# Kernel optimization log

Measured on AMD Instinct MI355X. Metric: run time of the kernel, lower is better.

Reference implementation:

```python
import jax, jax.numpy as jnp
import numpy as np

B, N, NODE_DIM = 8, 128, 64
L, RES_DIM = 512, 1024
CG, CP = 128, 128
NUM_GNN_STEPS = 3
HID = CG + CP // 2  # interaction hidden = 192


def setup_inputs() -> dict:
    key = jax.random.key(0)
    ks = jax.random.split(key, 20)
    a = (jax.random.uniform(ks[0], (B, N, N)) < 0.05).astype(jnp.float32)
    adj = jnp.clip(a + jnp.swapaxes(a, 1, 2), 0.0, 1.0)
    adj = adj * (1.0 - jnp.eye(N, dtype=jnp.float32))
    nodes = jax.random.normal(ks[1], (B, N, NODE_DIM), dtype=jnp.float32)
    prot = jax.random.normal(ks[2], (B, L, RES_DIM), dtype=jnp.float32)
    s = 0.02
    inp = {
        "adj_mats": adj, "nodes": nodes, "protein_sequences": prot,
        "Wn": jax.random.normal(ks[3], (NODE_DIM, CG)) * s, "bn": jnp.zeros((CG,)),
        "Wg": jax.random.normal(ks[4], (CG, CG)) * s, "bg": jnp.zeros((CG,)),
        "Wr": jax.random.normal(ks[5], (RES_DIM, CP)) * s, "br": jnp.zeros((CP,)),
        "Wa": jax.random.normal(ks[6], (CG + CP, 1)) * s, "ba": jnp.zeros((1,)),
        "W1": jax.random.normal(ks[7], (CG + CP, HID)) * s, "b1": jnp.zeros((HID,)),
        "W2": jax.random.normal(ks[8], (HID, CG)) * s, "b2": jnp.zeros((CG,)),
        "Wo": jax.random.normal(ks[9], (CG, 1)) * s, "bo": jnp.zeros((1,)),
    }
    return inp


def reference(adj_mats, nodes, protein_sequences,
              Wn, bn, Wg, bg, Wr, br, Wa, ba, W1, b1, W2, b2, Wo, bo):
    # node compression: [B,N,CG]
    h = nodes @ Wn + bn
    deg = jnp.clip(jnp.sum(adj_mats, axis=-1), 1.0, None)        # [B,N]
    norm = deg ** -0.5                                           # [B,N]
    for i in range(NUM_GNN_STEPS):
        m = jnp.einsum('bij,bjc->bic', adj_mats, h * norm[..., None])
        h = (m * norm[..., None]) @ Wg + bg
        h = jnp.tanh(h) if i == NUM_GNN_STEPS - 1 else jax.nn.relu(h)
    # residue compression: [B,L,CP]
    r = protein_sequences @ Wr + br
    # MergeSnE1: all-pairs broadcast concat -> [B, N*L, CG+CP]
    cat = jnp.concatenate([
        jnp.broadcast_to(h[:, :, None, :], (B, N, L, CG)),
        jnp.broadcast_to(r[:, None, :, :], (B, N, L, CP)),
    ], axis=-1).reshape(B, N * L, CG + CP)
    # attention: Linear -> Softmax over last dim (size 1 => all ones, faithful)
    attn = jax.nn.softmax(cat @ Wa + ba, axis=-1)                # [B,N*L,1]
    inter = jax.nn.relu(cat @ W1 + b1) @ W2 + b2                 # [B,N*L,CG]
    weighted_sum = jnp.sum(attn * inter, axis=1)                 # [B,CG]
    return weighted_sum @ Wo + bo                                # [B,1]
```

## Files before the change

kernel.cpp:

```cpp
#include <hip/hip_runtime.h>
#include <hip/hip_bf16.h>

#define BB 8
#define NN 128
#define ND 64
#define LL 512
#define RD 1024
#define CG 128
#define HID 192

typedef __attribute__((ext_vector_type(8))) short short8;
typedef __attribute__((ext_vector_type(4))) float f32x4;

__device__ __forceinline__ unsigned short f2bf(float x) {
    return __bfloat16_as_ushort(__float2bfloat16(x));
}
__device__ __forceinline__ float bf2f(unsigned short h) {
    unsigned u = ((unsigned)h) << 16;
    return __builtin_bit_cast(float, u);
}
__device__ __forceinline__ float fast_tanh(float x) {
    float e = __expf(2.0f * x);
    return 1.0f - 2.0f * __builtin_amdgcn_rcpf(e + 1.0f);
}
#define MFMA __builtin_amdgcn_mfma_f32_16x16x32_bf16

__global__ __launch_bounds__(512, 1) void k1(
    const float* __restrict__ Wr, const float* __restrict__ br,
    const float* __restrict__ W1, const float* __restrict__ b1,
    const float* __restrict__ Wg, const float* __restrict__ Wn,
    const float* __restrict__ W2, const float* __restrict__ b2,
    const float* __restrict__ Wo, const float* __restrict__ bo,
    unsigned short* __restrict__ WcT, float* __restrict__ vbuf,
    float* __restrict__ b1cg, float* __restrict__ out,
    unsigned short* __restrict__ WgTg, unsigned short* __restrict__ W1Tg,
    unsigned short* __restrict__ WnTg)
{
    __shared__ unsigned short W1T[HID][136];
    int t = threadIdx.x, blk = blockIdx.x;
    int w = t >> 6, l = t & 63, lr = l & 15, ks = l >> 4, lk = ks * 8;
    const float* W1b = W1 + CG * HID;

    if (blk < 16) {
        int r0 = blk * 64;
        #pragma unroll
        for (int q = 0; q < 48; ++q) {
            int e = t + 512 * q;
            int m = e / HID, c = e % HID;
            W1T[c][m] = f2bf(W1[(size_t)(CG + m) * HID + c]);
        }
        int rt = w & 3, jh = w >> 2;
        short8 awr[4];
        #pragma unroll
        for (int kk = 0; kk < 4; ++kk) {
            const float* wp = Wr + (size_t)(r0 + rt * 16 + lr) * CG + kk * 32 + lk;
            float4 q0 = *(const float4*)wp;
            float4 q1 = *(const float4*)(wp + 4);
            unsigned short u[8];
            u[0]=f2bf(q0.x); u[1]=f2bf(q0.y); u[2]=f2bf(q0.z); u[3]=f2bf(q0.w);
            u[4]=f2bf(q1.x); u[5]=f2bf(q1.y); u[6]=f2bf(q1.z); u[7]=f2bf(q1.w);
            awr[kk] = *(const short8*)u;
        }
        __syncthreads();
        #pragma unroll
        for (int jt6 = 0; jt6 < 6; ++jt6) {
            int jt = jh * 6 + jt6;
            f32x4 d = {0.f, 0.f, 0.f, 0.f};
            #pragma unroll
            for (int kk = 0; kk < 4; ++kk) {
                short8 bf = *(const short8*)(&W1T[jt * 16 + lr][kk * 32 + lk]);
                d = MFMA(awr[kk], bf, d, 0, 0, 0);
            }
            unsigned short u[4];
            #pragma unroll
            for (int i = 0; i < 4; ++i) u[i] = f2bf(d[i]);
            *(uint2*)(WcT + (size_t)(jt * 16 + lr) * RD + r0 + rt * 16 + ks * 4) = *(uint2*)u;
        }
        return;
    }
    if (blk == 16) {
        if (t < HID) {
            float s = 0.f;
            #pragma unroll 8
            for (int k = 0; k < CG; ++k) s = fmaf(W2[t * CG + k], Wo[k], s);
            vbuf[t] = s;
        }
        if (t < BB) {
            float s = 0.f;
            for (int k = 0; k < CG; ++k) s = fmaf(b2[k], Wo[k], s);
            out[t] = (float)(NN * LL) * s + bo[0];
        }
        if (t >= 192 && t < 384) {
            int j = t - 192;
            float s = b1[j];
            #pragma unroll 8
            for (int m = 0; m < CG; ++m)
                s = fmaf(br[m], W1b[(size_t)m * HID + j], s);
            b1cg[j] = s;
        }
        return;
    }
    if (blk < 21) {
        int c = (blk - 17) * 32 + (t >> 4);
        int j8 = (t & 15) * 8;
        unsigned short u[8];
        #pragma unroll
        for (int q = 0; q < 8; ++q)
            u[q] = f2bf(Wg[(size_t)(j8 + q) * CG + c]);
        *(short8*)(WgTg + (size_t)c * CG + j8) = *(const short8*)u;
        return;
    }
    if (blk < 24) {
        int jj0 = (blk - 21) * 64;
        #pragma unroll
        for (int qq = 0; qq < 2; ++qq) {
            int u8 = t + 512 * qq;
            int jj = jj0 + (u8 >> 4);
            int k8 = (u8 & 15) * 8;
            unsigned short u[8];
            #pragma unroll
            for (int q = 0; q < 8; ++q)
                u[q] = f2bf(W1[(size_t)(k8 + q) * HID + jj]);
            *(short8*)(W1Tg + (size_t)jj * CG + k8) = *(const short8*)u;
        }
        return;
    }
    #pragma unroll
    for (int qq = 0; qq < 2; ++qq) {
        int u8 = t + 512 * qq;
        int c = u8 >> 3;
        int k8 = (u8 & 7) * 8;
        unsigned short u[8];
        #pragma unroll
        for (int q = 0; q < 8; ++q)
            u[q] = f2bf(Wn[(size_t)(k8 + q) * CG + c]);
        *(short8*)(WnTg + (size_t)c * ND + k8) = *(const short8*)u;
    }
}

__global__ __launch_bounds__(512, 1) void k_gnn(
    const float* __restrict__ adj, const float* __restrict__ nodes,
    const unsigned short* __restrict__ WnTg, const float* __restrict__ bn,
    const unsigned short* __restrict__ WgTg, const float* __restrict__ bg,
    const unsigned short* __restrict__ W1Tg, const float* __restrict__ b1cg,
    unsigned short* __restrict__ hW1b)
{
    __shared__ unsigned short hT[NN][136];
    __shared__ unsigned short mbuf[NN][72];
    __shared__ unsigned short WgT[NN][136];
    __shared__ unsigned short W1T[HID][136];
    __shared__ float snorm[NN];
    __shared__ float b1cL[HID];
    __shared__ float sbg[NN];
    int t = threadIdx.x, blk = blockIdx.x;
    int w = t >> 6, l = t & 63, lr = l & 15, ks = l >> 4, lk = ks * 8;
    int b = blk;
    int i0 = w * 16;

    {
        float* dscr = (float*)&mbuf[0][0];
        int row = t >> 2, q4 = t & 3;
        const float* ar = adj + ((size_t)b * NN + row) * NN + q4 * 32;
        float d = 0.f;
        #pragma unroll
        for (int c4 = 0; c4 < 8; ++c4) {
            float4 p = *(const float4*)(ar + c4 * 4);
            d += (p.x + p.y) + (p.z + p.w);
        }
        dscr[row * 4 + q4] = d;
        __syncthreads();
        if (t < NN) {
            snorm[t] = rsqrtf(fmaxf(dscr[t*4] + dscr[t*4+1] + dscr[t*4+2] + dscr[t*4+3], 1.f));
        } else if (t < 320) {
            b1cL[t - 128] = b1cg[t - 128];
        } else if (t < 448) {
            sbg[t - 320] = bg[t - 320];
        }
        __syncthreads();
    }

    unsigned short* WnT = &mbuf[0][0];
    #pragma unroll
    for (int qq = 0; qq < 2; ++qq) {
        int u8 = t + 512 * qq;
        int c = u8 >> 3, k8 = (u8 & 7) * 8;
        *(short8*)(WnT + c * 72 + k8) = *(const short8*)(WnTg + (size_t)c * ND + k8);
    }
    #pragma unroll
    for (int qq = 0; qq < 4; ++qq) {
        int u8 = t + 512 * qq;
        int c = u8 >> 4, j8 = (u8 & 15) * 8;
        *(short8*)(&WgT[c][j8]) = *(const short8*)(WgTg + (size_t)c * CG + j8);
    }
    #pragma unroll
    for (int qq = 0; qq < 6; ++qq) {
        int u8 = t + 512 * qq;
        int jj = u8 >> 4, k8 = (u8 & 15) * 8;
        *(short8*)(&W1T[jj][k8]) = *(const short8*)(W1Tg + (size_t)jj * CG + k8);
    }

    short8 af[4];
    {
        float ni = snorm[i0 + lr];
        const float* ar = adj + ((size_t)b * NN + i0 + lr) * NN;
        #pragma unroll
        for (int kk = 0; kk < 4; ++kk) {
            int kb = kk * 32 + lk;
            float4 p0 = *(const float4*)(ar + kb);
            float4 p1 = *(const float4*)(ar + kb + 4);
            unsigned short u[8];
            u[0] = f2bf(p0.x * ni * snorm[kb+0]); u[1] = f2bf(p0.y * ni * snorm[kb+1]);
            u[2] = f2bf(p0.z * ni * snorm[kb+2]); u[3] = f2bf(p0.w * ni * snorm[kb+3]);
            u[4] = f2bf(p1.x * ni * snorm[kb+4]); u[5] = f2bf(p1.y * ni * snorm[kb+5]);
            u[6] = f2bf(p1.z * ni * snorm[kb+6]); u[7] = f2bf(p1.w * ni * snorm[kb+7]);
            af[kk] = *(const short8*)u;
        }
    }
    short8 bnod[2];
    #pragma unroll
    for (int kk = 0; kk < 2; ++kk) {
        const float* np = nodes + ((size_t)b * NN + i0 + lr) * ND + kk * 32 + lk;
        float4 q0 = *(const float4*)np;
        float4 q1 = *(const float4*)(np + 4);
        unsigned short u[8];
        u[0]=f2bf(q0.x); u[1]=f2bf(q0.y); u[2]=f2bf(q0.z); u[3]=f2bf(q0.w);
        u[4]=f2bf(q1.x); u[5]=f2bf(q1.y); u[6]=f2bf(q1.z); u[7]=f2bf(q1.w);
        bnod[kk] = *(const short8*)u;
    }
    __syncthreads();

    #pragma unroll
    for (int ct = 0; ct < 8; ++ct) {
        f32x4 d = {0.f, 0.f, 0.f, 0.f};
        #pragma unroll
        for (int kk = 0; kk < 2; ++kk) {
            short8 afw = *(const short8*)(WnT + (ct * 16 + lr) * 72 + kk * 32 + lk);
            d = MFMA(afw, bnod[kk], d, 0, 0, 0);
        }
        #pragma unroll
        for (int i = 0; i < 4; ++i)
            hT[ct * 16 + ks * 4 + i][i0 + lr] = f2bf(d[i] + bn[ct * 16 + ks * 4 + i]);
    }
    __syncthreads();

    for (int s = 0; s < 3; ++s) {
        f32x4 acc8[8];
        #pragma unroll
        for (int ct = 0; ct < 8; ++ct) acc8[ct] = (f32x4){0.f, 0.f, 0.f, 0.f};
        #pragma unroll
        for (int hf = 0; hf < 2; ++hf) {
            #pragma unroll
            for (int jt = 0; jt < 4; ++jt) {
                int jg = hf * 64 + jt * 16;
                f32x4 d = {0.f, 0.f, 0.f, 0.f};
                #pragma unroll
                for (int kk = 0; kk < 4; ++kk) {
                    short8 bf = *(const short8*)(&hT[jg + lr][kk * 32 + lk]);
                    d = MFMA(af[kk], bf, d, 0, 0, 0);
                }
                #pragma unroll
                for (int i = 0; i < 4; ++i)
                    mbuf[i0 + ks * 4 + i][jt * 16 + lr] = f2bf(d[i]);
            }
            short8 bm[2];
            #pragma unroll
            for (int kk = 0; kk < 2; ++kk)
                bm[kk] = *(const short8*)(&mbuf[i0 + lr][kk * 32 + lk]);
            #pragma unroll
            for (int ct = 0; ct < 8; ++ct) {
                #pragma unroll
                for (int kk = 0; kk < 2; ++kk) {
                    short8 wf = *(const short8*)(&WgT[ct * 16 + lr][hf * 64 + kk * 32 + lk]);
                    if (s < 2)
                        acc8[ct] = MFMA(wf, bm[kk], acc8[ct], 0, 0, 0);
                    else
                        acc8[ct] = MFMA(bm[kk], wf, acc8[ct], 0, 0, 0);
                }
            }
        }
        __syncthreads();
        if (s < 2) {
            #pragma unroll
            for (int ct = 0; ct < 8; ++ct)
                #pragma unroll
                for (int i = 0; i < 4; ++i)
                    hT[ct * 16 + ks * 4 + i][i0 + lr] =
                        f2bf(fmaxf(acc8[ct][i] + sbg[ct * 16 + ks * 4 + i], 0.f));
        } else {
            #pragma unroll
            for (int ct = 0; ct < 8; ++ct)
                #pragma unroll
                for (int i = 0; i < 4; ++i)
                    hT[i0 + ks * 4 + i][ct * 16 + lr] =
                        f2bf(fast_tanh(acc8[ct][i] + sbg[ct * 16 + lr]));
        }
        __syncthreads();
    }

    {
        short8 bh[4];
        #pragma unroll
        for (int kk = 0; kk < 4; ++kk)
            bh[kk] = *(const short8*)(&hT[i0 + lr][kk * 32 + lk]);
        #pragma unroll
        for (int jjt = 0; jjt < 12; ++jjt) {
            f32x4 d = {0.f, 0.f, 0.f, 0.f};
            #pragma unroll
            for (int kk = 0; kk < 4; ++kk) {
                short8 wf = *(const short8*)(&W1T[jjt * 16 + lr][kk * 32 + lk]);
                d = MFMA(wf, bh[kk], d, 0, 0, 0);
            }
            #pragma unroll
            for (int i = 0; i < 4; ++i) {
                int jj = jjt * 16 + ks * 4 + i;
                hW1b[(size_t)b * HID * NN + jj * NN + i0 + lr] = f2bf(d[i] + b1cL[jj]);
            }
        }
    }
}

__global__ __launch_bounds__(512, 4) void k_gemm(
    const float* __restrict__ prot, const unsigned short* __restrict__ WcT,
    const unsigned short* __restrict__ hW1b, const float* __restrict__ vbuf,
    float* __restrict__ out)
{
    __shared__ unsigned short aT[16 * 1032];
    __shared__ unsigned short h1[HID * 136];
    __shared__ float pbuf[2 * 16 * 192];
    __shared__ float sred[8];
    int t = threadIdx.x, blk = blockIdx.x;
    int b = blk >> 5, lc = blk & 31;
    int w = t >> 6, l = t & 63, lr = l & 15, ks = l >> 4, lk = ks * 8;
    int w2 = w >> 2, wj = w & 3;

    #pragma unroll
    for (int q = 0; q < 4; ++q) {
        int e = t + 512 * q;
        int row = e >> 7;
        int c8 = (e & 127) * 8;
        const float* pr = prot + ((size_t)(b * LL + lc * 16 + row)) * RD + c8;
        float4 p0 = *(const float4*)pr;
        float4 p1 = *(const float4*)(pr + 4);
        unsigned short u[8];
        u[0]=f2bf(p0.x); u[1]=f2bf(p0.y); u[2]=f2bf(p0.z); u[3]=f2bf(p0.w);
        u[4]=f2bf(p1.x); u[5]=f2bf(p1.y); u[6]=f2bf(p1.z); u[7]=f2bf(p1.w);
        *(short8*)(aT + row * 1032 + c8) = *(const short8*)u;
    }
    #pragma unroll
    for (int q = 0; q < 6; ++q) {
        int u8 = t + 512 * q;
        int row = u8 >> 4;
        int n8 = (u8 & 15) * 8;
        short8 v = *(const short8*)(hW1b + (size_t)b * HID * NN + row * NN + n8);
        *(short8*)(h1 + row * 136 + n8) = v;
    }
    float v0 = vbuf[wj * 48 + lr];
    float v1 = vbuf[wj * 48 + 16 + lr];
    float v2 = vbuf[wj * 48 + 32 + lr];
    __syncthreads();

    f32x4 a0 = {0.f,0.f,0.f,0.f}, a1 = a0, a2 = a0;
    {
        const unsigned short* ap = aT + lr * 1032 + w2 * 512 + lk;
        const unsigned short* bp = WcT + (size_t)(wj * 48 + lr) * RD + w2 * 512 + lk;
        #pragma unroll 4
        for (int k0 = 0; k0 < 512; k0 += 32) {
            short8 av = *(const short8*)(ap + k0);
            short8 b0 = *(const short8*)(bp + k0);
            short8 b1 = *(const short8*)(bp + 16 * RD + k0);
            short8 b2 = *(const short8*)(bp + 32 * RD + k0);
            a0 = MFMA(av, b0, a0, 0, 0, 0);
            a1 = MFMA(av, b1, a1, 0, 0, 0);
            a2 = MFMA(av, b2, a2, 0, 0, 0);
        }
    }
    #pragma unroll
    for (int i = 0; i < 4; ++i) {
        int r = ks * 4 + i;
        pbuf[(w2 * 16 + r) * 192 + wj * 48 + lr]      = a0[i];
        pbuf[(w2 * 16 + r) * 192 + wj * 48 + 16 + lr] = a1[i];
        pbuf[(w2 * 16 + r) * 192 + wj * 48 + 32 + lr] = a2[i];
    }
    __syncthreads();
    float rw0[4], rw1[4], rw2[4];
    #pragma unroll
    for (int i = 0; i < 4; ++i) {
        int r = ks * 4 + i;
        rw0[i] = pbuf[r * 192 + wj*48 + lr]      + pbuf[(16 + r) * 192 + wj*48 + lr];
        rw1[i] = pbuf[r * 192 + wj*48 + 16 + lr] + pbuf[(16 + r) * 192 + wj*48 + 16 + lr];
        rw2[i] = pbuf[r * 192 + wj*48 + 32 + lr] + pbuf[(16 + r) * 192 + wj*48 + 32 + lr];
    }

    const unsigned short* h0p = h1 + (wj * 48 + lr) * 136 + w2 * 64;
    const unsigned short* h1p = h0p + 16 * 136;
    const unsigned short* h2p = h0p + 32 * 136;
    float s = 0.f;
    #pragma unroll 2
    for (int n0 = 0; n0 < 64; n0 += 4) {
        unsigned short e0[4], e1[4], e2[4];
        *(uint2*)e0 = *(const uint2*)(h0p + n0);
        *(uint2*)e1 = *(const uint2*)(h1p + n0);
        *(uint2*)e2 = *(const uint2*)(h2p + n0);
        #pragma unroll
        for (int q = 0; q < 4; ++q) {
            float hh0 = bf2f(e0[q]), hh1 = bf2f(e1[q]), hh2 = bf2f(e2[q]);
            #pragma unroll
            for (int i = 0; i < 4; ++i) {
                s = fmaf(v0, fmaxf(rw0[i] + hh0, 0.f), s);
                s = fmaf(v1, fmaxf(rw1[i] + hh1, 0.f), s);
                s = fmaf(v2, fmaxf(rw2[i] + hh2, 0.f), s);
            }
        }
    }
    for (int off = 32; off; off >>= 1) s += __shfl_down(s, off);
    if (l == 0) sred[w] = s;
    __syncthreads();
    if (t == 0) {
        float tot = ((sred[0] + sred[1]) + (sred[2] + sred[3]))
                  + ((sred[4] + sred[5]) + (sred[6] + sred[7]));
        atomicAdd(&out[b], tot);
    }
}

extern "C" void kernel_launch(void* const* d_in, const int* in_sizes, int n_in,
                              void* d_out, int out_size, void* d_ws, size_t ws_size,
                              hipStream_t stream)
{
    const float* adj   = (const float*)d_in[0];
    const float* nodes = (const float*)d_in[1];
    const float* prot  = (const float*)d_in[2];
    const float* Wn    = (const float*)d_in[3];
    const float* bn    = (const float*)d_in[4];
    const float* Wg    = (const float*)d_in[5];
    const float* bg    = (const float*)d_in[6];
    const float* Wr    = (const float*)d_in[7];
    const float* br    = (const float*)d_in[8];
    const float* W1    = (const float*)d_in[11];
    const float* b1    = (const float*)d_in[12];
    const float* W2    = (const float*)d_in[13];
    const float* b2    = (const float*)d_in[14];
    const float* Wo    = (const float*)d_in[15];
    const float* bo    = (const float*)d_in[16];

    float* ws     = (float*)d_ws;
    float* vbuf   = ws;
    float* b1cg   = ws + 192;
    unsigned short* hW1b = (unsigned short*)(ws + 384);
    unsigned short* WcT  = hW1b + (size_t)BB * HID * NN;
    unsigned short* WgTg = WcT + (size_t)HID * RD;
    unsigned short* W1Tg = WgTg + CG * CG;
    unsigned short* WnTg = W1Tg + HID * CG;
    float* out    = (float*)d_out;

    hipLaunchKernelGGL(k1, dim3(25), dim3(512), 0, stream,
                       Wr, br, W1, b1, Wg, Wn, W2, b2, Wo, bo,
                       WcT, vbuf, b1cg, out, WgTg, W1Tg, WnTg);
    hipLaunchKernelGGL(k_gnn, dim3(8), dim3(512), 0, stream,
                       adj, nodes, WnTg, bn, WgTg, bg, W1Tg, b1cg, hW1b);
    hipLaunchKernelGGL(k_gemm, dim3(256), dim3(512), 0, stream,
                       prot, WcT, hW1b, vbuf, out);
}
```

Baseline: 56.69 us.

## Merge GNN and projection GEMM kernels with flag-based inter-block synchronization

Fuses the GNN kernel and the protein GEMM kernel into one 256-block launch. Blocks 248-255 run the GNN per batch and publish a release flag. The other blocks first compute their protein projection tiles, with blocks 0-7 also taking the tiles normally owned by the GNN blocks, then spin on the flag before consuming hW1b. The aim is to overlap the serial GNN with the bandwidth-heavy GEMM and drop one launch. The cost is spin-waiting, a dependence on all blocks being co-resident to avoid deadlock, and a heavier load on blocks 0-7.

Result: slower. 70.35 us (+24.1%).

```diff
diff --git a/kernel.cpp b/kernel.cpp
--- a/kernel.cpp
+++ b/kernel.cpp
@@ -34,7 +34,7 @@
     unsigned short* __restrict__ WcT, float* __restrict__ vbuf,
     float* __restrict__ b1cg, float* __restrict__ out,
     unsigned short* __restrict__ WgTg, unsigned short* __restrict__ W1Tg,
-    unsigned short* __restrict__ WnTg)
+    unsigned short* __restrict__ WnTg, unsigned* __restrict__ flags)
 {
     __shared__ unsigned short W1T[HID][136];
     int t = threadIdx.x, blk = blockIdx.x;
@@ -98,6 +98,7 @@
                 s = fmaf(br[m], W1b[(size_t)m * HID + j], s);
             b1cg[j] = s;
         }
+        if (t >= 384) flags[t - 384] = 0u;
         return;
     }
     if (blk < 21) {
@@ -138,201 +139,9 @@
     }
 }
 
-__global__ __launch_bounds__(512, 1) void k_gnn(
-    const float* __restrict__ adj, const float* __restrict__ nodes,
-    const unsigned short* __restrict__ WnTg, const float* __restrict__ bn,
-    const unsigned short* __restrict__ WgTg, const float* __restrict__ bg,
-    const unsigned short* __restrict__ W1Tg, const float* __restrict__ b1cg,
-    unsigned short* __restrict__ hW1b)
-{
-    __shared__ unsigned short hT[NN][136];
-    __shared__ unsigned short mbuf[NN][72];
-    __shared__ unsigned short WgT[NN][136];
-    __shared__ unsigned short W1T[HID][136];
-    __shared__ float snorm[NN];
-    __shared__ float b1cL[HID];
-    __shared__ float sbg[NN];
-    int t = threadIdx.x, blk = blockIdx.x;
-    int w = t >> 6, l = t & 63, lr = l & 15, ks = l >> 4, lk = ks * 8;
-    int b = blk;
-    int i0 = w * 16;
-
-    {
-        float* dscr = (float*)&mbuf[0][0];
-        int row = t >> 2, q4 = t & 3;
-        const float* ar = adj + ((size_t)b * NN + row) * NN + q4 * 32;
-        float d = 0.f;
-        #pragma unroll
-        for (int c4 = 0; c4 < 8; ++c4) {
-            float4 p = *(const float4*)(ar + c4 * 4);
-            d += (p.x + p.y) + (p.z + p.w);
-        }
-        dscr[row * 4 + q4] = d;
-        __syncthreads();
-        if (t < NN) {
-            snorm[t] = rsqrtf(fmaxf(dscr[t*4] + dscr[t*4+1] + dscr[t*4+2] + dscr[t*4+3], 1.f));
-        } else if (t < 320) {
-            b1cL[t - 128] = b1cg[t - 128];
-        } else if (t < 448) {
-            sbg[t - 320] = bg[t - 320];
-        }
-        __syncthreads();
-    }
-
-    unsigned short* WnT = &mbuf[0][0];
-    #pragma unroll
-    for (int qq = 0; qq < 2; ++qq) {
-        int u8 = t + 512 * qq;
-        int c = u8 >> 3, k8 = (u8 & 7) * 8;
-        *(short8*)(WnT + c * 72 + k8) = *(const short8*)(WnTg + (size_t)c * ND + k8);
-    }
-    #pragma unroll
-    for (int qq = 0; qq < 4; ++qq) {
-        int u8 = t + 512 * qq;
-        int c = u8 >> 4, j8 = (u8 & 15) * 8;
-        *(short8*)(&WgT[c][j8]) = *(const short8*)(WgTg + (size_t)c * CG + j8);
-    }
-    #pragma unroll
-    for (int qq = 0; qq < 6; ++qq) {
-        int u8 = t + 512 * qq;
-        int jj = u8 >> 4, k8 = (u8 & 15) * 8;
-        *(short8*)(&W1T[jj][k8]) = *(const short8*)(W1Tg + (size_t)jj * CG + k8);
-    }
-
-    short8 af[4];
-    {
-        float ni = snorm[i0 + lr];
-        const float* ar = adj + ((size_t)b * NN + i0 + lr) * NN;
-        #pragma unroll
-        for (int kk = 0; kk < 4; ++kk) {
-            int kb = kk * 32 + lk;
-            float4 p0 = *(const float4*)(ar + kb);
-            float4 p1 = *(const float4*)(ar + kb + 4);
-            unsigned short u[8];
-            u[0] = f2bf(p0.x * ni * snorm[kb+0]); u[1] = f2bf(p0.y * ni * snorm[kb+1]);
-            u[2] = f2bf(p0.z * ni * snorm[kb+2]); u[3] = f2bf(p0.w * ni * snorm[kb+3]);
-            u[4] = f2bf(p1.x * ni * snorm[kb+4]); u[5] = f2bf(p1.y * ni * snorm[kb+5]);
-            u[6] = f2bf(p1.z * ni * snorm[kb+6]); u[7] = f2bf(p1.w * ni * snorm[kb+7]);
-            af[kk] = *(const short8*)u;
-        }
-    }
-    short8 bnod[2];
-    #pragma unroll
-    for (int kk = 0; kk < 2; ++kk) {
-        const float* np = nodes + ((size_t)b * NN + i0 + lr) * ND + kk * 32 + lk;
-        float4 q0 = *(const float4*)np;
-        float4 q1 = *(const float4*)(np + 4);
-        unsigned short u[8];
-        u[0]=f2bf(q0.x); u[1]=f2bf(q0.y); u[2]=f2bf(q0.z); u[3]=f2bf(q0.w);
-        u[4]=f2bf(q1.x); u[5]=f2bf(q1.y); u[6]=f2bf(q1.z); u[7]=f2bf(q1.w);
-        bnod[kk] = *(const short8*)u;
-    }
-    __syncthreads();
-
-    #pragma unroll
-    for (int ct = 0; ct < 8; ++ct) {
-        f32x4 d = {0.f, 0.f, 0.f, 0.f};
-        #pragma unroll
-        for (int kk = 0; kk < 2; ++kk) {
-            short8 afw = *(const short8*)(WnT + (ct * 16 + lr) * 72 + kk * 32 + lk);
-            d = MFMA(afw, bnod[kk], d, 0, 0, 0);
-        }
-        #pragma unroll
-        for (int i = 0; i < 4; ++i)
-            hT[ct * 16 + ks * 4 + i][i0 + lr] = f2bf(d[i] + bn[ct * 16 + ks * 4 + i]);
-    }
-    __syncthreads();
-
-    for (int s = 0; s < 3; ++s) {
-        f32x4 acc8[8];
-        #pragma unroll
-        for (int ct = 0; ct < 8; ++ct) acc8[ct] = (f32x4){0.f, 0.f, 0.f, 0.f};
-        #pragma unroll
-        for (int hf = 0; hf < 2; ++hf) {
-            #pragma unroll
-            for (int jt = 0; jt < 4; ++jt) {
-                int jg = hf * 64 + jt * 16;
-                f32x4 d = {0.f, 0.f, 0.f, 0.f};
-                #pragma unroll
-                for (int kk = 0; kk < 4; ++kk) {
-                    short8 bf = *(const short8*)(&hT[jg + lr][kk * 32 + lk]);
-                    d = MFMA(af[kk], bf, d, 0, 0, 0);
-                }
-                #pragma unroll
-                for (int i = 0; i < 4; ++i)
-                    mbuf[i0 + ks * 4 + i][jt * 16 + lr] = f2bf(d[i]);
-            }
-            short8 bm[2];
-            #pragma unroll
-            for (int kk = 0; kk < 2; ++kk)
-                bm[kk] = *(const short8*)(&mbuf[i0 + lr][kk * 32 + lk]);
-            #pragma unroll
-            for (int ct = 0; ct < 8; ++ct) {
-                #pragma unroll
-                for (int kk = 0; kk < 2; ++kk) {
-                    short8 wf = *(const short8*)(&WgT[ct * 16 + lr][hf * 64 + kk * 32 + lk]);
-                    if (s < 2)
-                        acc8[ct] = MFMA(wf, bm[kk], acc8[ct], 0, 0, 0);
-                    else
-                        acc8[ct] = MFMA(bm[kk], wf, acc8[ct], 0, 0, 0);
-                }
-            }
-        }
-        __syncthreads();
-        if (s < 2) {
-            #pragma unroll
-            for (int ct = 0; ct < 8; ++ct)
-                #pragma unroll
-                for (int i = 0; i < 4; ++i)
-                    hT[ct * 16 + ks * 4 + i][i0 + lr] =
-                        f2bf(fmaxf(acc8[ct][i] + sbg[ct * 16 + ks * 4 + i], 0.f));
-        } else {
-            #pragma unroll
-            for (int ct = 0; ct < 8; ++ct)
-                #pragma unroll
-                for (int i = 0; i < 4; ++i)
-                    hT[i0 + ks * 4 + i][ct * 16 + lr] =
-                        f2bf(fast_tanh(acc8[ct][i] + sbg[ct * 16 + lr]));
-        }
-        __syncthreads();
-    }
-
-    {
-        short8 bh[4];
-        #pragma unroll
-        for (int kk = 0; kk < 4; ++kk)
-            bh[kk] = *(const short8*)(&hT[i0 + lr][kk * 32 + lk]);
-        #pragma unroll
-        for (int jjt = 0; jjt < 12; ++jjt) {
-            f32x4 d = {0.f, 0.f, 0.f, 0.f};
-            #pragma unroll
-            for (int kk = 0; kk < 4; ++kk) {
-                short8 wf = *(const short8*)(&W1T[jjt * 16 + lr][kk * 32 + lk]);
-                d = MFMA(wf, bh[kk], d, 0, 0, 0);
-            }
-            #pragma unroll
-            for (int i = 0; i < 4; ++i) {
-                int jj = jjt * 16 + ks * 4 + i;
-                hW1b[(size_t)b * HID * NN + jj * NN + i0 + lr] = f2bf(d[i] + b1cL[jj]);
-            }
-        }
-    }
-}
-
-__global__ __launch_bounds__(512, 4) void k_gemm(
-    const float* __restrict__ prot, const unsigned short* __restrict__ WcT,
-    const unsigned short* __restrict__ hW1b, const float* __restrict__ vbuf,
-    float* __restrict__ out)
-{
-    __shared__ unsigned short aT[16 * 1032];
-    __shared__ unsigned short h1[HID * 136];
-    __shared__ float pbuf[2 * 16 * 192];
-    __shared__ float sred[8];
-    int t = threadIdx.x, blk = blockIdx.x;
-    int b = blk >> 5, lc = blk & 31;
-    int w = t >> 6, l = t & 63, lr = l & 15, ks = l >> 4, lk = ks * 8;
-    int w2 = w >> 2, wj = w & 3;
-
+__device__ __forceinline__ void stage_aT(
+    unsigned short* aT, const float* __restrict__ prot, int b, int lc, int t)
+{
     #pragma unroll
     for (int q = 0; q < 4; ++q) {
         int e = t + 512 * q;
@@ -346,6 +155,47 @@
         u[4]=f2bf(p1.x); u[5]=f2bf(p1.y); u[6]=f2bf(p1.z); u[7]=f2bf(p1.w);
         *(short8*)(aT + row * 1032 + c8) = *(const short8*)u;
     }
+}
+
+__device__ __forceinline__ void gemm_combine(
+    const unsigned short* aT, float* pbuf,
+    const unsigned short* __restrict__ WcT,
+    int lr, int lk, int ks, int w2, int wj,
+    float rw0[4], float rw1[4], float rw2[4])
+{
+    f32x4 a0 = {0.f,0.f,0.f,0.f}, a1 = a0, a2 = a0;
+    const unsigned short* ap = aT + lr * 1032 + w2 * 512 + lk;
+    const unsigned short* bp = WcT + (size_t)(wj * 48 + lr) * RD + w2 * 512 + lk;
+    #pragma unroll 4
+    for (int k0 = 0; k0 < 512; k0 += 32) {
+        short8 av = *(const short8*)(ap + k0);
+        short8 b0 = *(const short8*)(bp + k0);
+        short8 b1 = *(const short8*)(bp + 16 * RD + k0);
+        short8 b2 = *(const short8*)(bp + 32 * RD + k0);
+        a0 = MFMA(av, b0, a0, 0, 0, 0);
+        a1 = MFMA(av, b1, a1, 0, 0, 0);
+        a2 = MFMA(av, b2, a2, 0, 0, 0);
+    }
+    #pragma unroll
+    for (int i = 0; i < 4; ++i) {
+        int r = ks * 4 + i;
+        pbuf[(w2 * 16 + r) * 192 + wj * 48 + lr]      = a0[i];
+        pbuf[(w2 * 16 + r) * 192 + wj * 48 + 16 + lr] = a1[i];
+        pbuf[(w2 * 16 + r) * 192 + wj * 48 + 32 + lr] = a2[i];
+    }
+    __syncthreads();
+    #pragma unroll
+    for (int i = 0; i < 4; ++i) {
+        int r = ks * 4 + i;
+        rw0[i] = pbuf[r * 192 + wj*48 + lr]      + pbuf[(16 + r) * 192 + wj*48 + lr];
+        rw1[i] = pbuf[r * 192 + wj*48 + 16 + lr] + pbuf[(16 + r) * 192 + wj*48 + 16 + lr];
+        rw2[i] = pbuf[r * 192 + wj*48 + 32 + lr] + pbuf[(16 + r) * 192 + wj*48 + 32 + lr];
+    }
+}
+
+__device__ __forceinline__ void stage_h1(
+    unsigned short* h1, const unsigned short* __restrict__ hW1b, int b, int t)
+{
     #pragma unroll
     for (int q = 0; q < 6; ++q) {
         int u8 = t + 512 * q;
@@ -354,43 +204,15 @@
         short8 v = *(const short8*)(hW1b + (size_t)b * HID * NN + row * NN + n8);
         *(short8*)(h1 + row * 136 + n8) = v;
     }
-    float v0 = vbuf[wj * 48 + lr];
-    float v1 = vbuf[wj * 48 + 16 + lr];
-    float v2 = vbuf[wj * 48 + 32 + lr];
-    __syncthreads();
-
-    f32x4 a0 = {0.f,0.f,0.f,0.f}, a1 = a0, a2 = a0;
-    {
-        const unsigned short* ap = aT + lr * 1032 + w2 * 512 + lk;
-        const unsigned short* bp = WcT + (size_t)(wj * 48 + lr) * RD + w2 * 512 + lk;
-        #pragma unroll 4
-        for (int k0 = 0; k0 < 512; k0 += 32) {
-            short8 av = *(const short8*)(ap + k0);
-            short8 b0 = *(const short8*)(bp + k0);
-            short8 b1 = *(const short8*)(bp + 16 * RD + k0);
-            short8 b2 = *(const short8*)(bp + 32 * RD + k0);
-            a0 = MFMA(av, b0, a0, 0, 0, 0);
-            a1 = MFMA(av, b1, a1, 0, 0, 0);
-            a2 = MFMA(av, b2, a2, 0, 0, 0);
-        }
-    }
-    #pragma unroll
-    for (int i = 0; i < 4; ++i) {
-        int r = ks * 4 + i;
-        pbuf[(w2 * 16 + r) * 192 + wj * 48 + lr]      = a0[i];
-        pbuf[(w2 * 16 + r) * 192 + wj * 48 + 16 + lr] = a1[i];
-        pbuf[(w2 * 16 + r) * 192 + wj * 48 + 32 + lr] = a2[i];
-    }
-    __syncthreads();
-    float rw0[4], rw1[4], rw2[4];
-    #pragma unroll
-    for (int i = 0; i < 4; ++i) {
-        int r = ks * 4 + i;
-        rw0[i] = pbuf[r * 192 + wj*48 + lr]      + pbuf[(16 + r) * 192 + wj*48 + lr];
-        rw1[i] = pbuf[r * 192 + wj*48 + 16 + lr] + pbuf[(16 + r) * 192 + wj*48 + 16 + lr];
-        rw2[i] = pbuf[r * 192 + wj*48 + 32 + lr] + pbuf[(16 + r) * 192 + wj*48 + 32 + lr];
-    }
-
+}
+
+__device__ __forceinline__ void epilogue(
+    const unsigned short* h1, float* sred,
+    const float rw0[4], const float rw1[4], const float rw2[4],
+    float v0, float v1, float v2,
+    int b, int w, int l, int lr, int w2, int wj, int t,
+    float* __restrict__ out)
+{
     const unsigned short* h0p = h1 + (wj * 48 + lr) * 136 + w2 * 64;
     const unsigned short* h1p = h0p + 16 * 136;
     const unsigned short* h2p = h0p + 32 * 136;
@@ -419,6 +241,253 @@
         float tot = ((sred[0] + sred[1]) + (sred[2] + sred[3]))
                   + ((sred[4] + sred[5]) + (sred[6] + sred[7]));
         atomicAdd(&out[b], tot);
+    }
+}
+
+__global__ __launch_bounds__(512, 1) void kmerged(
+    const float* __restrict__ adj, const float* __restrict__ nodes,
+    const unsigned short* __restrict__ WnTg, const float* __restrict__ bn,
+    const unsigned short* __restrict__ WgTg, const float* __restrict__ bg,
+    const unsigned short* __restrict__ W1Tg, const float* __restrict__ b1cg,
+    unsigned short* __restrict__ hW1b,
+    const float* __restrict__ prot, const unsigned short* __restrict__ WcT,
+    const float* __restrict__ vbuf, float* __restrict__ out,
+    unsigned* __restrict__ flags)
+{
+    __shared__ __align__(16) char pool[142080];
+    __shared__ float sred[8];
+    int t = threadIdx.x, blk = blockIdx.x;
+    int w = t >> 6, l = t & 63, lr = l & 15, ks = l >> 4, lk = ks * 8;
+
+    if (blk >= 248) {
+        unsigned short (*hT)[136]  = (unsigned short(*)[136])(pool);
+        unsigned short (*mbuf)[72] = (unsigned short(*)[72])(pool + 34816);
+        unsigned short (*WgT)[136] = (unsigned short(*)[136])(pool + 53248);
+        unsigned short (*W1T)[136] = (unsigned short(*)[136])(pool + 88064);
+        float* snorm = (float*)(pool + 140288);
+        float* b1cL  = (float*)(pool + 140800);
+        float* sbg   = (float*)(pool + 141568);
+        int b = blk - 248;
+        int i0 = w * 16;
+
+        {
+            float* dscr = (float*)&mbuf[0][0];
+            int row = t >> 2, q4 = t & 3;
+            const float* ar = adj + ((size_t)b * NN + row) * NN + q4 * 32;
+            float d = 0.f;
+            #pragma unroll
+            for (int c4 = 0; c4 < 8; ++c4) {
+                float4 p = *(const float4*)(ar + c4 * 4);
+                d += (p.x + p.y) + (p.z + p.w);
+            }
+            dscr[row * 4 + q4] = d;
+            __syncthreads();
+            if (t < NN) {
+                snorm[t] = rsqrtf(fmaxf(dscr[t*4] + dscr[t*4+1] + dscr[t*4+2] + dscr[t*4+3], 1.f));
+            } else if (t < 320) {
+                b1cL[t - 128] = b1cg[t - 128];
+            } else if (t < 448) {
+                sbg[t - 320] = bg[t - 320];
+            }
+            __syncthreads();
+        }
+
+        unsigned short* WnT = &mbuf[0][0];
+        #pragma unroll
+        for (int qq = 0; qq < 2; ++qq) {
+            int u8 = t + 512 * qq;
+            int c = u8 >> 3, k8 = (u8 & 7) * 8;
+            *(short8*)(WnT + c * 72 + k8) = *(const short8*)(WnTg + (size_t)c * ND + k8);
+        }
+        #pragma unroll
+        for (int qq = 0; qq < 4; ++qq) {
+            int u8 = t + 512 * qq;
+            int c = u8 >> 4, j8 = (u8 & 15) * 8;
+            *(short8*)(&WgT[c][j8]) = *(const short8*)(WgTg + (size_t)c * CG + j8);
+        }
+        #pragma unroll
+        for (int qq = 0; qq < 6; ++qq) {
+            int u8 = t + 512 * qq;
+            int jj = u8 >> 4, k8 = (u8 & 15) * 8;
+            *(short8*)(&W1T[jj][k8]) = *(const short8*)(W1Tg + (size_t)jj * CG + k8);
+        }
+
+        short8 af[4];
+        {
+            float ni = snorm[i0 + lr];
+            const float* ar = adj + ((size_t)b * NN + i0 + lr) * NN;
+            #pragma unroll
+            for (int kk = 0; kk < 4; ++kk) {
+                int kb = kk * 32 + lk;
+                float4 p0 = *(const float4*)(ar + kb);
+                float4 p1 = *(const float4*)(ar + kb + 4);
+                unsigned short u[8];
+                u[0] = f2bf(p0.x * ni * snorm[kb+0]); u[1] = f2bf(p0.y * ni * snorm[kb+1]);
+                u[2] = f2bf(p0.z * ni * snorm[kb+2]); u[3] = f2bf(p0.w * ni * snorm[kb+3]);
+                u[4] = f2bf(p1.x * ni * snorm[kb+4]); u[5] = f2bf(p1.y * ni * snorm[kb+5]);
+                u[6] = f2bf(p1.z * ni * snorm[kb+6]); u[7] = f2bf(p1.w * ni * snorm[kb+7]);
+                af[kk] = *(const short8*)u;
+            }
+        }
+        short8 bnod[2];
+        #pragma unroll
+        for (int kk = 0; kk < 2; ++kk) {
+            const float* np = nodes + ((size_t)b * NN + i0 + lr) * ND + kk * 32 + lk;
+            float4 q0 = *(const float4*)np;
+            float4 q1 = *(const float4*)(np + 4);
+            unsigned short u[8];
+            u[0]=f2bf(q0.x); u[1]=f2bf(q0.y); u[2]=f2bf(q0.z); u[3]=f2bf(q0.w);
+            u[4]=f2bf(q1.x); u[5]=f2bf(q1.y); u[6]=f2bf(q1.z); u[7]=f2bf(q1.w);
+            bnod[kk] = *(const short8*)u;
+        }
+        __syncthreads();
+
+        #pragma unroll
+        for (int ct = 0; ct < 8; ++ct) {
+            f32x4 d = {0.f, 0.f, 0.f, 0.f};
+            #pragma unroll
+            for (int kk = 0; kk < 2; ++kk) {
+                short8 afw = *(const short8*)(WnT + (ct * 16 + lr) * 72 + kk * 32 + lk);
+                d = MFMA(afw, bnod[kk], d, 0, 0, 0);
+            }
+            #pragma unroll
+            for (int i = 0; i < 4; ++i)
+                hT[ct * 16 + ks * 4 + i][i0 + lr] = f2bf(d[i] + bn[ct * 16 + ks * 4 + i]);
+        }
+        __syncthreads();
+
+        for (int s = 0; s < 3; ++s) {
+            f32x4 acc8[8];
+            #pragma unroll
+            for (int ct = 0; ct < 8; ++ct) acc8[ct] = (f32x4){0.f, 0.f, 0.f, 0.f};
+            #pragma unroll
+            for (int hf = 0; hf < 2; ++hf) {
+                #pragma unroll
+                for (int jt = 0; jt < 4; ++jt) {
+                    int jg = hf * 64 + jt * 16;
+                    f32x4 d = {0.f, 0.f, 0.f, 0.f};
+                    #pragma unroll
+                    for (int kk = 0; kk < 4; ++kk) {
+                        short8 bf = *(const short8*)(&hT[jg + lr][kk * 32 + lk]);
+                        d = MFMA(af[kk], bf, d, 0, 0, 0);
+                    }
+                    #pragma unroll
+                    for (int i = 0; i < 4; ++i)
+                        mbuf[i0 + ks * 4 + i][jt * 16 + lr] = f2bf(d[i]);
+                }
+                short8 bm[2];
+                #pragma unroll
+                for (int kk = 0; kk < 2; ++kk)
+                    bm[kk] = *(const short8*)(&mbuf[i0 + lr][kk * 32 + lk]);
+                #pragma unroll
+                for (int ct = 0; ct < 8; ++ct) {
+                    #pragma unroll
+                    for (int kk = 0; kk < 2; ++kk) {
+                        short8 wf = *(const short8*)(&WgT[ct * 16 + lr][hf * 64 + kk * 32 + lk]);
+                        if (s < 2)
+                            acc8[ct] = MFMA(wf, bm[kk], acc8[ct], 0, 0, 0);
+                        else
+                            acc8[ct] = MFMA(bm[kk], wf, acc8[ct], 0, 0, 0);
+                    }
+                }
+            }
+            __syncthreads();
+            if (s < 2) {
+                #pragma unroll
+                for (int ct = 0; ct < 8; ++ct)
+                    #pragma unroll
+                    for (int i = 0; i < 4; ++i)
+                        hT[ct * 16 + ks * 4 + i][i0 + lr] =
+                            f2bf(fmaxf(acc8[ct][i] + sbg[ct * 16 + ks * 4 + i], 0.f));
+            } else {
+                #pragma unroll
+                for (int ct = 0; ct < 8; ++ct)
+                    #pragma unroll
+                    for (int i = 0; i < 4; ++i)
+                        hT[i0 + ks * 4 + i][ct * 16 + lr] =
+                            f2bf(fast_tanh(acc8[ct][i] + sbg[ct * 16 + lr]));
+            }
+            __syncthreads();
+        }
+
+        {
+            short8 bh[4];
+            #pragma unroll
+            for (int kk = 0; kk < 4; ++kk)
+                bh[kk] = *(const short8*)(&hT[i0 + lr][kk * 32 + lk]);
+            #pragma unroll
+            for (int jjt = 0; jjt < 12; ++jjt) {
+                f32x4 d = {0.f, 0.f, 0.f, 0.f};
+                #pragma unroll
+                for (int kk = 0; kk < 4; ++kk) {
+                    short8 wf = *(const short8*)(&W1T[jjt * 16 + lr][kk * 32 + lk]);
+                    d = MFMA(wf, bh[kk], d, 0, 0, 0);
+                }
+                #pragma unroll
+                for (int i = 0; i < 4; ++i) {
+                    int jj = jjt * 16 + ks * 4 + i;
+                    hW1b[(size_t)b * HID * NN + jj * NN + i0 + lr] = f2bf(d[i] + b1cL[jj]);
+                }
+            }
+        }
+        __syncthreads();
+        if (t == 0) {
+            __threadfence();
+            __hip_atomic_store(&flags[b * 16], 1u, __ATOMIC_RELEASE,
+                               __HIP_MEMORY_SCOPE_AGENT);
+        }
+        return;
+    }
+
+    unsigned short* aT = (unsigned short*)pool;
+    float* pbuf = (float*)(pool + 33024);
+    unsigned short* h1 = (unsigned short*)(pool + 57600);
+    int w2 = w >> 2, wj = w & 3;
+    int b1_ = blk >> 5, lc1 = blk & 31;
+    int have2 = (blk < 8);
+    int ti2 = 248 + blk;
+    int b2_ = ti2 >> 5, lc2 = ti2 & 31;
+
+    float v0 = vbuf[wj * 48 + lr];
+    float v1 = vbuf[wj * 48 + 16 + lr];
+    float v2 = vbuf[wj * 48 + 32 + lr];
+
+    float rwA0[4], rwA1[4], rwA2[4];
+    float rwB0[4], rwB1[4], rwB2[4];
+
+    stage_aT(aT, prot, b1_, lc1, t);
+    __syncthreads();
+    gemm_combine(aT, pbuf, WcT, lr, lk, ks, w2, wj, rwA0, rwA1, rwA2);
+    if (have2) {
+        __syncthreads();
+        stage_aT(aT, prot, b2_, lc2, t);
+        __syncthreads();
+        gemm_combine(aT, pbuf, WcT, lr, lk, ks, w2, wj, rwB0, rwB1, rwB2);
+    }
+
+    if (t == 0) {
+        while (__hip_atomic_load(&flags[b1_ * 16], __ATOMIC_ACQUIRE,
+                                 __HIP_MEMORY_SCOPE_AGENT) == 0u)
+            __builtin_amdgcn_s_sleep(16);
+        __threadfence();
+    }
+    __syncthreads();
+    stage_h1(h1, hW1b, b1_, t);
+    __syncthreads();
+    epilogue(h1, sred, rwA0, rwA1, rwA2, v0, v1, v2, b1_, w, l, lr, w2, wj, t, out);
+
+    if (have2) {
+        __syncthreads();
+        if (t == 0) {
+            while (__hip_atomic_load(&flags[b2_ * 16], __ATOMIC_ACQUIRE,
+                                     __HIP_MEMORY_SCOPE_AGENT) == 0u)
+                __builtin_amdgcn_s_sleep(16);
+            __threadfence();
+        }
+        __syncthreads();
+        stage_h1(h1, hW1b, b2_, t);
+        __syncthreads();
+        epilogue(h1, sred, rwB0, rwB1, rwB2, v0, v1, v2, b2_, w, l, lr, w2, wj, t, out);
     }
 }
 
@@ -445,7 +514,8 @@
     float* ws     = (float*)d_ws;
     float* vbuf   = ws;
     float* b1cg   = ws + 192;
-    unsigned short* hW1b = (unsigned short*)(ws + 384);
+    unsigned* flags = (unsigned*)(ws + 384);
+    unsigned short* hW1b = (unsigned short*)(ws + 512);
     unsigned short* WcT  = hW1b + (size_t)BB * HID * NN;
     unsigned short* WgTg = WcT + (size_t)HID * RD;
     unsigned short* W1Tg = WgTg + CG * CG;
@@ -454,9 +524,8 @@
 
     hipLaunchKernelGGL(k1, dim3(25), dim3(512), 0, stream,
                        Wr, br, W1, b1, Wg, Wn, W2, b2, Wo, bo,
-                       WcT, vbuf, b1cg, out, WgTg, W1Tg, WnTg);
-    hipLaunchKernelGGL(k_gnn, dim3(8), dim3(512), 0, stream,
-                       adj, nodes, WnTg, bn, WgTg, bg, W1Tg, b1cg, hW1b);
-    hipLaunchKernelGGL(k_gemm, dim3(256), dim3(512), 0, stream,
-                       prot, WcT, hW1b, vbuf, out);
-}
+                       WcT, vbuf, b1cg, out, WgTg, W1Tg, WnTg, flags);
+    hipLaunchKernelGGL(kmerged, dim3(256), dim3(512), 0, stream,
+                       adj, nodes, WnTg, bn, WgTg, bg, W1Tg, b1cg, hW1b,
+                       prot, WcT, vbuf, out, flags);
+}
```
